# Kernel optimization log

Hardware: AMD Instinct MI355X
Metric: run time of the kernel (lower is better)

The kernel has to match this reference:

```python
import jax, jax.numpy as jnp
import numpy as np

B, T, D, H, L, FF, SPLIT = 2, 4096, 256, 4 * 0 + 8, 4, 1024, 2048
HD = D // H
EPS = 1e-5


def _layernorm(x, s, b):
    mu = jnp.mean(x, axis=-1, keepdims=True)
    var = jnp.mean(jnp.square(x - mu), axis=-1, keepdims=True)
    return (x - mu) * jax.lax.rsqrt(var + EPS) * s + b


def setup_inputs() -> dict:
    key = jax.random.key(0)
    ks = jax.random.split(key, 10)
    sc = 0.02
    inp = {
        "rows": jax.random.normal(ks[0], (B, T, D), jnp.float32),
        "train_target_embeddings": jax.random.normal(ks[1], (B, SPLIT, D), jnp.float32),
        "Wq": sc * jax.random.normal(ks[2], (L, D, D), jnp.float32),
        "bq": jnp.zeros((L, D), jnp.float32),
        "Wk": sc * jax.random.normal(ks[3], (L, D, D), jnp.float32),
        "bk": jnp.zeros((L, D), jnp.float32),
        "Wv": sc * jax.random.normal(ks[4], (L, D, D), jnp.float32),
        "bv": jnp.zeros((L, D), jnp.float32),
        "Wo": sc * jax.random.normal(ks[5], (L, D, D), jnp.float32),
        "bo": jnp.zeros((L, D), jnp.float32),
        "W1": sc * jax.random.normal(ks[6], (L, D, FF), jnp.float32),
        "b1": jnp.zeros((L, FF), jnp.float32),
        "W2": sc * jax.random.normal(ks[7], (L, FF, D), jnp.float32),
        "b2": jnp.zeros((L, D), jnp.float32),
        "ln1_s": jnp.ones((L, D), jnp.float32),
        "ln1_b": jnp.zeros((L, D), jnp.float32),
        "ln2_s": jnp.ones((L, D), jnp.float32),
        "ln2_b": jnp.zeros((L, D), jnp.float32),
        "split": SPLIT,
    }
    return inp


def reference(rows, train_target_embeddings, Wq, bq, Wk, bk, Wv, bv, Wo, bo,
              W1, b1, W2, b2, ln1_s, ln1_b, ln2_s, ln2_b, split):
    # residual add of train target embeddings onto the train rows
    x = rows.at[:, :split, :].add(train_target_embeddings)
    t = x.shape[1]
    # allowed mask: every query can see all train columns; test queries also see themselves
    key_is_train = jnp.arange(t) < split                      # [T]
    allowed = key_is_train[None, :] | jnp.eye(t, dtype=bool)  # [T,T]
    neg = jnp.asarray(-1e9, x.dtype)
    scale = 1.0 / np.sqrt(HD)
    n_layers = Wq.shape[0]
    for l in range(n_layers):
        # multi-head attention with structured mask
        q = (x @ Wq[l] + bq[l]).reshape(x.shape[0], t, H, HD)
        k = (x @ Wk[l] + bk[l]).reshape(x.shape[0], t, H, HD)
        v = (x @ Wv[l] + bv[l]).reshape(x.shape[0], t, H, HD)
        logits = jnp.einsum('bqhd,bkhd->bhqk', q, k) * scale
        logits = jnp.where(allowed[None, None], logits, neg)
        attn = jax.nn.softmax(logits, axis=-1)
        o = jnp.einsum('bhqk,bkhd->bqhd', attn, v).reshape(x.shape[0], t, D)
        x = _layernorm(x + (o @ Wo[l] + bo[l]), ln1_s[l], ln1_b[l])
        # feed-forward
        h = jax.nn.gelu(x @ W1[l] + b1[l])
        x = _layernorm(x + (h @ W2[l] + b2[l]), ln2_s[l], ln2_b[l])
    return x
```

## Files before the change

### kernel.cpp

```cpp
#include <hip/hip_runtime.h>
#include <cstdint>
#include <cstddef>

#define TSEQ 4096
#define BATCH 2
#define DIM 256
#define NHEAD 8
#define HDIM 32
#define NLAYER 4
#define FFDIM 1024
#define SPLITN 2048
#define MROWS (BATCH * TSEQ)

#define QSCALE 0.2550784545f

typedef __attribute__((ext_vector_type(4))) float f32x4;
typedef __attribute__((ext_vector_type(8))) short bf16x8;

__device__ __forceinline__ short f2bf(float f) {
  union { float f; uint32_t u; } v; v.f = f;
  uint32_t r = v.u + 0x7fffu + ((v.u >> 16) & 1u);
  return (short)(r >> 16);
}

__device__ __forceinline__ float fast_exp2(float x) {
#if __has_builtin(__builtin_amdgcn_exp2f)
  return __builtin_amdgcn_exp2f(x);
#else
  float r;
  asm volatile("v_exp_f32 %0, %1\n\ts_nop 1" : "=v"(r) : "v"(x));
  return r;
#endif
}

__device__ __forceinline__ uint32_t pack2bf(float a, float b) {
  union { float f; uint32_t u; } ua, ub; ua.f = a; ub.f = b;
  return ((ua.u + 0x8000u) >> 16) | ((ub.u + 0x8000u) & 0xffff0000u);
}

__device__ __forceinline__ float gelu_f(float x) {
  float u = 0.7978845608f * x * (1.0f + 0.044715f * x * x);
  u = fminf(fmaxf(u, -20.f), 20.f);
  float e = fast_exp2(2.885390082f * u);
  float t = (e - 1.0f) / (e + 1.0f);
  return 0.5f * x * (1.0f + t);
}

#define AS1 __attribute__((address_space(1)))
#define AS3 __attribute__((address_space(3)))
__device__ __forceinline__ void gload16(const void* g, void* l) {
  __builtin_amdgcn_global_load_lds((AS1 void*)g, (AS3 void*)l, 16, 0, 0);
}

__global__ __launch_bounds__(256) void prep_w(
    const float* __restrict__ Wq, const float* __restrict__ Wk,
    const float* __restrict__ Wv, const float* __restrict__ Wo,
    const float* __restrict__ W1, const float* __restrict__ W2,
    short* __restrict__ qkvT, short* __restrict__ woT,
    short* __restrict__ w1T, short* __restrict__ w2T)
{
  const int NQKV = NLAYER * 768 * DIM;
  const int NO   = NLAYER * DIM * DIM;
  const int NF   = NLAYER * FFDIM * DIM;
  const int total = NQKV + NO + 2 * NF;
  for (int idx = blockIdx.x * 256 + threadIdx.x; idx < total; idx += gridDim.x * 256) {
    if (idx < NQKV) {
      const int l = idx / (768 * DIM);
      const int rem = idx - l * 768 * DIM;
      const int n = rem >> 8, k = rem & 255;
      const float* src = (n < 256) ? Wq : ((n < 512) ? Wk : Wv);
      qkvT[idx] = f2bf(src[((size_t)l * DIM + k) * DIM + (n & 255)]);
    } else if (idx < NQKV + NO) {
      const int j = idx - NQKV;
      const int l = j >> 16;
      const int rem = j & 65535;
      const int n = rem >> 8, k = rem & 255;
      woT[j] = f2bf(Wo[((size_t)l * DIM + k) * DIM + n]);
    } else if (idx < NQKV + NO + NF) {
      const int j = idx - NQKV - NO;
      const int l = j >> 18;
      const int rem = j & 262143;
      const int n = rem >> 8, k = rem & 255;
      w1T[j] = f2bf(W1[((size_t)l * DIM + k) * FFDIM + n]);
    } else {
      const int j = idx - NQKV - NO - NF;
      const int l = j >> 18;
      const int rem = j & 262143;
      const int n = rem >> 10, k = rem & 1023;
      w2T[j] = f2bf(W2[((size_t)l * FFDIM + k) * DIM + n]);
    }
  }
}

__global__ __launch_bounds__(256) void prep_x(
    const float* __restrict__ rows, const float* __restrict__ tte,
    float* __restrict__ xf, short* __restrict__ xb)
{
  const size_t idx = (size_t)blockIdx.x * 256 + threadIdx.x;
  float4 v = ((const float4*)rows)[idx];
  const size_t e = idx * 4;
  const int m = (int)(e >> 8);
  const int d = (int)(e & 255);
  const int t = m & (TSEQ - 1);
  const int bb = m >> 12;
  if (t < SPLITN) {
    const float4 a = ((const float4*)tte)[((size_t)bb * SPLITN + t) * (DIM / 4) + (d >> 2)];
    v.x += a.x; v.y += a.y; v.z += a.z; v.w += a.w;
  }
  ((float4*)xf)[idx] = v;
  short4 pk; pk.x = f2bf(v.x); pk.y = f2bf(v.y); pk.z = f2bf(v.z); pk.w = f2bf(v.w);
  ((short4*)xb)[idx] = pk;
}

#define GBM 128
#define GBN 64
#define GBK 64

template<int EPI>
__global__ __launch_bounds__(256, 4) void gemm_bt(
    const short* __restrict__ A, const short* __restrict__ BT,
    const float* __restrict__ bias0, const float* __restrict__ bias1,
    const float* __restrict__ bias2, void* __restrict__ Cout,
    int M, int N, int K)
{
  __shared__ short As[GBM * GBK];
  __shared__ short Bs[GBN * GBK];
  const int tid = threadIdx.x;
  const int lane = tid & 63;
  const int wave = tid >> 6;
  const int wm = wave & 1, wn = wave >> 1;
  const int col = lane & 15, quad = lane >> 4;

  const short* Ab = A + (size_t)blockIdx.x * GBM * K;
  const short* Bb = BT + (size_t)blockIdx.y * GBN * K;

  const f32x4 fz = {0.f, 0.f, 0.f, 0.f};
  f32x4 acc[4][2];
#pragma unroll
  for (int i = 0; i < 4; ++i)
#pragma unroll
    for (int j = 0; j < 2; ++j) acc[i][j] = fz;

  for (int k0 = 0; k0 < K; k0 += GBK) {
#pragma unroll
    for (int p = 0; p < 4; ++p) {
      int i = p * 256 + tid;
      gload16(Ab + (size_t)(i >> 3) * K + k0 + (i & 7) * 8, &As[i * 8]);
    }
#pragma unroll
    for (int p = 0; p < 2; ++p) {
      int i = p * 256 + tid;
      gload16(Bb + (size_t)(i >> 3) * K + k0 + (i & 7) * 8, &Bs[i * 8]);
    }
    __syncthreads();
#pragma unroll
    for (int ks = 0; ks < GBK; ks += 32) {
      bf16x8 af[4], bfr[2];
#pragma unroll
      for (int tm = 0; tm < 4; ++tm)
        af[tm] = *(const bf16x8*)&As[(wm * 64 + tm * 16 + col) * GBK + ks + quad * 8];
#pragma unroll
      for (int tn = 0; tn < 2; ++tn)
        bfr[tn] = *(const bf16x8*)&Bs[(wn * 32 + tn * 16 + col) * GBK + ks + quad * 8];
#pragma unroll
      for (int tm = 0; tm < 4; ++tm)
#pragma unroll
        for (int tn = 0; tn < 2; ++tn)
          acc[tm][tn] = __builtin_amdgcn_mfma_f32_16x16x32_bf16(af[tm], bfr[tn], acc[tm][tn], 0, 0, 0);
    }
    __syncthreads();
  }

#pragma unroll
  for (int tm = 0; tm < 4; ++tm) {
    const int mbase = blockIdx.x * GBM + wm * 64 + tm * 16 + quad * 4;
#pragma unroll
    for (int tn = 0; tn < 2; ++tn) {
      const int n = blockIdx.y * GBN + wn * 32 + tn * 16 + col;
      float bv;
      if (EPI == 1) bv = (n < 256) ? bias0[n] : ((n < 512) ? bias1[n - 256] : bias2[n - 512]);
      else          bv = bias0[n];
#pragma unroll
      for (int r = 0; r < 4; ++r) {
        float v = acc[tm][tn][r] + bv;
        size_t off = (size_t)(mbase + r) * N + n;
        if (EPI == 1) {
          if (n < 256) v *= QSCALE;
          ((short*)Cout)[off] = f2bf(v);
        } else {
          ((short*)Cout)[off] = f2bf(gelu_f(v));
        }
      }
    }
  }
}

__global__ __launch_bounds__(256, 3) void gemm_ln(
    const short* __restrict__ A, const short* __restrict__ BT,
    const float* __restrict__ bias, const float* __restrict__ xres,
    const float* __restrict__ gs, const float* __restrict__ gb,
    float* __restrict__ xoutf, short* __restrict__ xoutb, int K)
{
  __shared__ short As[32 * 64];
  __shared__ short Bs[256 * 64];
  __shared__ float ssum[4][32], ssq[4][32];
  const int tid = threadIdx.x;
  const int lane = tid & 63;
  const int wave = tid >> 6;
  const int col = lane & 15, quad = lane >> 4;
  const int m0 = blockIdx.x * 32;
  const short* Ab = A + (size_t)m0 * K;

  const f32x4 fz = {0.f, 0.f, 0.f, 0.f};
  f32x4 acc[2][4];
#pragma unroll
  for (int i = 0; i < 2; ++i)
#pragma unroll
    for (int j = 0; j < 4; ++j) acc[i][j] = fz;

  for (int k0 = 0; k0 < K; k0 += 64) {
    gload16(Ab + (size_t)(tid >> 3) * K + k0 + (tid & 7) * 8, &As[tid * 8]);
#pragma unroll
    for (int p = 0; p < 8; ++p) {
      int i = p * 256 + tid;
      gload16(BT + (size_t)(i >> 3) * K + k0 + (i & 7) * 8, &Bs[i * 8]);
    }
    __syncthreads();
#pragma unroll
    for (int ks = 0; ks < 64; ks += 32) {
      bf16x8 af[2], bfr[4];
#pragma unroll
      for (int tm = 0; tm < 2; ++tm)
        af[tm] = *(const bf16x8*)&As[(tm * 16 + col) * 64 + ks + quad * 8];
#pragma unroll
      for (int tn = 0; tn < 4; ++tn)
        bfr[tn] = *(const bf16x8*)&Bs[(wave * 64 + tn * 16 + col) * 64 + ks + quad * 8];
#pragma unroll
      for (int tm = 0; tm < 2; ++tm)
#pragma unroll
        for (int tn = 0; tn < 4; ++tn)
          acc[tm][tn] = __builtin_amdgcn_mfma_f32_16x16x32_bf16(af[tm], bfr[tn], acc[tm][tn], 0, 0, 0);
    }
    __syncthreads();
  }

  const float* resb = xres + (size_t)m0 * DIM;
#pragma unroll
  for (int tn = 0; tn < 4; ++tn) {
    const int n = wave * 64 + tn * 16 + col;
    const float bv = bias[n];
#pragma unroll
    for (int tm = 0; tm < 2; ++tm)
#pragma unroll
      for (int r = 0; r < 4; ++r) {
        const int row = tm * 16 + quad * 4 + r;
        acc[tm][tn][r] += bv + resb[(size_t)row * DIM + n];
      }
  }

#pragma unroll
  for (int tm = 0; tm < 2; ++tm)
#pragma unroll
    for (int r = 0; r < 4; ++r) {
      float s = 0.f, q = 0.f;
#pragma unroll
      for (int tn = 0; tn < 4; ++tn) { const float v = acc[tm][tn][r]; s += v; q += v * v; }
      s += __shfl_xor(s, 1); q += __shfl_xor(q, 1);
      s += __shfl_xor(s, 2); q += __shfl_xor(q, 2);
      s += __shfl_xor(s, 4); q += __shfl_xor(q, 4);
      s += __shfl_xor(s, 8); q += __shfl_xor(q, 8);
      if (col == 0) { const int row = tm * 16 + quad * 4 + r; ssum[wave][row] = s; ssq[wave][row] = q; }
    }
  __syncthreads();
  if (tid < 32) {
    const float S = ssum[0][tid] + ssum[1][tid] + ssum[2][tid] + ssum[3][tid];
    const float Q = ssq[0][tid] + ssq[1][tid] + ssq[2][tid] + ssq[3][tid];
    const float mu = S * (1.0f / DIM);
    const float var = Q * (1.0f / DIM) - mu * mu;
    ssum[0][tid] = mu;
    ssq[0][tid] = rsqrtf(var + 1e-5f);
  }
  __syncthreads();

#pragma unroll
  for (int tm = 0; tm < 2; ++tm)
#pragma unroll
    for (int tn = 0; tn < 4; ++tn) {
      const int n = wave * 64 + tn * 16 + col;
      const float g = gs[n], bb = gb[n];
#pragma unroll
      for (int r = 0; r < 4; ++r) {
        const int row = tm * 16 + quad * 4 + r;
        const float out = (acc[tm][tn][r] - ssum[0][row]) * ssq[0][row] * g + bb;
        xoutf[(size_t)(m0 + row) * DIM + n] = out;
        xoutb[(size_t)(m0 + row) * DIM + n] = f2bf(out);
      }
    }
}

__global__ __launch_bounds__(256) void transpose_v(
    const short* __restrict__ qkv, short* __restrict__ vt)
{
  __shared__ short tile[32][33];
  const int t0 = blockIdx.x * 32;
  const int c0 = blockIdx.y * 32;
  const int b = blockIdx.z;
  const int tx = threadIdx.x & 31, ty = threadIdx.x >> 5;
#pragma unroll
  for (int i = 0; i < 4; ++i) {
    const int t = t0 + ty + i * 8;
    tile[ty + i * 8][tx] = qkv[(size_t)(b * TSEQ + t) * 768 + 512 + c0 + tx];
  }
  __syncthreads();
#pragma unroll
  for (int i = 0; i < 4; ++i) {
    const int c = c0 + ty + i * 8;
    vt[(size_t)(b * DIM + c) * TSEQ + t0 + tx] = tile[tx][ty + i * 8];
  }
}

#define AKT 64
#define KSPL 1024

__global__ __launch_bounds__(256, 4) void attn_kernel(
    const short* __restrict__ qkv, const short* __restrict__ vt,
    float* __restrict__ Opart, float* __restrict__ lpart)
{
  __shared__ short Kbuf[2][AKT * HDIM];
  __shared__ short Vbuf[2][HDIM * AKT];
  __shared__ short Pall[4][32][72];

  const int tid = threadIdx.x;
  const int lane = tid & 63;
  const int wave = tid >> 6;
  const int col = lane & 15, quad = lane >> 4;
  const int bh = blockIdx.y;
  const int b = bh >> 3, h = bh & 7;
  const int hz = blockIdx.z;
  const int q0 = blockIdx.x * 128 + wave * 32;

  short (*P)[72] = Pall[wave];

  const short* qbase = qkv + (size_t)b * TSEQ * 768 + h * HDIM;
  const short* kbase = qbase + 256;
  const short* vtb = vt + (size_t)bh * HDIM * TSEQ;

  const short* ksrc = kbase + (size_t)(hz * KSPL + (tid & 63)) * 768 + (tid >> 6) * 8;
  const short* vsrc = vtb + (size_t)(tid >> 3) * TSEQ + hz * KSPL + (((tid & 7) ^ ((tid >> 3) & 7)) * 8);

  const bf16x8 qf0 = *(const bf16x8*)(qbase + (size_t)(q0 + col) * 768 + quad * 8);
  const bf16x8 qf1 = *(const bf16x8*)(qbase + (size_t)(q0 + 16 + col) * 768 + quad * 8);

  bf16x8 ones;
#pragma unroll
  for (int i = 0; i < 8; ++i) ones[i] = (short)0x3F80;

  const f32x4 fz = {0.f, 0.f, 0.f, 0.f};
  f32x4 o[2][2] = {{fz, fz}, {fz, fz}};
  f32x4 lacc0 = fz, lacc1 = fz;

  gload16(ksrc, &Kbuf[0][tid * 8]);
  gload16(vsrc, &Vbuf[0][tid * 8]);

  int cur = 0;
  for (int t = 0; t < KSPL / AKT; ++t) {
    __syncthreads();
    if (t + 1 < KSPL / AKT) {
      const int kn = (t + 1) * AKT;
      gload16(ksrc + (size_t)kn * 768, &Kbuf[1 - cur][tid * 8]);
      gload16(vsrc + kn, &Vbuf[1 - cur][tid * 8]);
    }
    const short* kb = Kbuf[cur];
    const short* vb = Vbuf[cur];

#pragma unroll
    for (int st = 0; st < 4; ++st) {
      const bf16x8 kf = *(const bf16x8*)&kb[(quad * 64 + st * 16 + col) * 8];
      const f32x4 s0 = __builtin_amdgcn_mfma_f32_16x16x32_bf16(kf, qf0, fz, 0, 0, 0);
      const f32x4 s1 = __builtin_amdgcn_mfma_f32_16x16x32_bf16(kf, qf1, fz, 0, 0, 0);
      uint2 w0, w1;
      w0.x = pack2bf(fast_exp2(s0[0]), fast_exp2(s0[1]));
      w0.y = pack2bf(fast_exp2(s0[2]), fast_exp2(s0[3]));
      w1.x = pack2bf(fast_exp2(s1[0]), fast_exp2(s1[1]));
      w1.y = pack2bf(fast_exp2(s1[2]), fast_exp2(s1[3]));
      *(uint2*)&P[col][st * 16 + quad * 4] = w0;
      *(uint2*)&P[16 + col][st * 16 + quad * 4] = w1;
    }
    asm volatile("s_waitcnt lgkmcnt(0)" ::: "memory");

#pragma unroll
    for (int kh = 0; kh < 2; ++kh) {
      const bf16x8 pf0 = *(const bf16x8*)&P[col][kh * 32 + quad * 8];
      const bf16x8 pf1 = *(const bf16x8*)&P[16 + col][kh * 32 + quad * 8];
#pragma unroll
      for (int hh = 0; hh < 2; ++hh) {
        const int hd = hh * 16 + col;
        const bf16x8 vf = *(const bf16x8*)&vb[hd * AKT + (((kh * 4 + quad) ^ (hd & 7)) * 8)];
        o[0][hh] = __builtin_amdgcn_mfma_f32_16x16x32_bf16(pf0, vf, o[0][hh], 0, 0, 0);
        o[1][hh] = __builtin_amdgcn_mfma_f32_16x16x32_bf16(pf1, vf, o[1][hh], 0, 0, 0);
      }
      lacc0 = __builtin_amdgcn_mfma_f32_16x16x32_bf16(pf0, ones, lacc0, 0, 0, 0);
      lacc1 = __builtin_amdgcn_mfma_f32_16x16x32_bf16(pf1, ones, lacc1, 0, 0, 0);
    }
    cur ^= 1;
  }

  if (hz == 1 && blockIdx.x >= SPLITN / 128) {
#pragma unroll
    for (int qsub = 0; qsub < 2; ++qsub) {
      const int qd = q0 + qsub * 16;
      const bf16x8 qf = qsub ? qf1 : qf0;
      const bf16x8 kf = *(const bf16x8*)(kbase + (size_t)(qd + col) * 768 + quad * 8);
      const f32x4 sd = __builtin_amdgcn_mfma_f32_16x16x32_bf16(kf, qf, fz, 0, 0, 0);
      float pd[4];
#pragma unroll
      for (int r = 0; r < 4; ++r)
        pd[r] = (quad * 4 + r) == col ? fast_exp2(sd[r]) : 0.f;
      uint2 w0, wz; wz.x = 0; wz.y = 0;
      w0.x = pack2bf(pd[0], pd[1]); w0.y = pack2bf(pd[2], pd[3]);
      *(uint2*)&P[qsub * 16 + col][quad * 4] = w0;
      *(uint2*)&P[qsub * 16 + col][16 + quad * 4] = wz;
    }
    asm volatile("s_waitcnt lgkmcnt(0)" ::: "memory");
#pragma unroll
    for (int qsub = 0; qsub < 2; ++qsub) {
      const int qd = q0 + qsub * 16;
      const bf16x8 pf = *(const bf16x8*)&P[qsub * 16 + col][quad * 8];
#pragma unroll
      for (int hh = 0; hh < 2; ++hh) {
        const bf16x8 vf = *(const bf16x8*)(vtb + (size_t)(hh * 16 + col) * TSEQ + qd + quad * 8);
        o[qsub][hh] = __builtin_amdgcn_mfma_f32_16x16x32_bf16(pf, vf, o[qsub][hh], 0, 0, 0);
      }
      if (qsub == 0) lacc0 = __builtin_amdgcn_mfma_f32_16x16x32_bf16(pf, ones, lacc0, 0, 0, 0);
      else           lacc1 = __builtin_amdgcn_mfma_f32_16x16x32_bf16(pf, ones, lacc1, 0, 0, 0);
    }
  }

  float* Ob = Opart + (size_t)hz * MROWS * DIM;
  float* lb = lpart + (size_t)hz * 16 * TSEQ + (size_t)bh * TSEQ;
#pragma unroll
  for (int qsub = 0; qsub < 2; ++qsub) {
    const f32x4 la = qsub ? lacc1 : lacc0;
    const int qq = q0 + qsub * 16 + quad * 4;
    const int rowb = b * TSEQ + qq;
#pragma unroll
    for (int r = 0; r < 4; ++r) {
      if (col == 0) lb[qq + r] = la[r];
#pragma unroll
      for (int hh = 0; hh < 2; ++hh)
        Ob[(size_t)(rowb + r) * DIM + h * HDIM + hh * 16 + col] = o[qsub][hh][r];
    }
  }
}

__global__ __launch_bounds__(256) void attn_combine(
    const float* __restrict__ Opart, const float* __restrict__ lpart,
    short* __restrict__ ob)
{
  const int idx4 = blockIdx.x * 256 + threadIdx.x;
  const int row = idx4 >> 6, d4 = idx4 & 63;
  const int h = d4 >> 3, b = row >> 12, t = row & (TSEQ - 1);
  const int bh = b * 8 + h;
  const float l = lpart[bh * TSEQ + t] + lpart[16 * TSEQ + bh * TSEQ + t];
  const float4 o0 = ((const float4*)Opart)[idx4];
  const float4 o1 = ((const float4*)Opart)[(size_t)MROWS * (DIM / 4) + idx4];
  const float linv = 1.0f / l;
  short4 pk;
  pk.x = f2bf((o0.x + o1.x) * linv);
  pk.y = f2bf((o0.y + o1.y) * linv);
  pk.z = f2bf((o0.z + o1.z) * linv);
  pk.w = f2bf((o0.w + o1.w) * linv);
  ((short4*)ob)[idx4] = pk;
}

extern "C" void kernel_launch(void* const* d_in, const int* in_sizes, int n_in,
                              void* d_out, int out_size, void* d_ws, size_t ws_size,
                              hipStream_t stream)
{
  const float* rows = (const float*)d_in[0];
  const float* tte  = (const float*)d_in[1];
  const float* Wq = (const float*)d_in[2];  const float* bq = (const float*)d_in[3];
  const float* Wk = (const float*)d_in[4];  const float* bk = (const float*)d_in[5];
  const float* Wv = (const float*)d_in[6];  const float* bv = (const float*)d_in[7];
  const float* Wo = (const float*)d_in[8];  const float* bo = (const float*)d_in[9];
  const float* W1 = (const float*)d_in[10]; const float* b1 = (const float*)d_in[11];
  const float* W2 = (const float*)d_in[12]; const float* b2 = (const float*)d_in[13];
  const float* ln1s = (const float*)d_in[14]; const float* ln1b = (const float*)d_in[15];
  const float* ln2s = (const float*)d_in[16]; const float* ln2b = (const float*)d_in[17];

  char* p = (char*)d_ws;
  float* xf   = (float*)p;  p += (size_t)MROWS * DIM * 4;
  short* xb   = (short*)p;  p += (size_t)MROWS * DIM * 2;
  short* qkv  = (short*)p;  p += (size_t)MROWS * 768 * 2;
  short* vtb  = (short*)p;  p += (size_t)BATCH * DIM * TSEQ * 2;
  short* ob   = (short*)p;  p += (size_t)MROWS * DIM * 2;
  short* hb   = (short*)p;  p += (size_t)MROWS * FFDIM * 2;
  float* Opart = (float*)p; p += (size_t)2 * MROWS * DIM * 4;
  float* lpart = (float*)p; p += (size_t)2 * 16 * TSEQ * 4;
  short* qkvT = (short*)p;  p += (size_t)NLAYER * 768 * DIM * 2;
  short* woT  = (short*)p;  p += (size_t)NLAYER * DIM * DIM * 2;
  short* w1T  = (short*)p;  p += (size_t)NLAYER * FFDIM * DIM * 2;
  short* w2T  = (short*)p;  p += (size_t)NLAYER * DIM * FFDIM * 2;

  prep_w<<<2048, 256, 0, stream>>>(Wq, Wk, Wv, Wo, W1, W2, qkvT, woT, w1T, w2T);
  prep_x<<<MROWS * DIM / 4 / 256, 256, 0, stream>>>(rows, tte, xf, xb);

  for (int l = 0; l < NLAYER; ++l) {
    gemm_bt<1><<<dim3(MROWS / GBM, 768 / GBN), 256, 0, stream>>>(
        xb, qkvT + (size_t)l * 768 * DIM, bq + l * DIM, bk + l * DIM, bv + l * DIM,
        qkv, MROWS, 768, DIM);
    transpose_v<<<dim3(TSEQ / 32, DIM / 32, BATCH), 256, 0, stream>>>(qkv, vtb);
    attn_kernel<<<dim3(TSEQ / 128, BATCH * NHEAD, 2), 256, 0, stream>>>(qkv, vtb, Opart, lpart);
    attn_combine<<<MROWS * DIM / 4 / 256, 256, 0, stream>>>(Opart, lpart, ob);
    gemm_ln<<<MROWS / 32, 256, 0, stream>>>(
        ob, woT + (size_t)l * DIM * DIM, bo + l * DIM, xf,
        ln1s + l * DIM, ln1b + l * DIM, xf, xb, DIM);
    gemm_bt<3><<<dim3(MROWS / GBM, FFDIM / GBN), 256, 0, stream>>>(
        xb, w1T + (size_t)l * FFDIM * DIM, b1 + l * FFDIM, nullptr, nullptr,
        hb, MROWS, FFDIM, DIM);
    float* xo = (l == NLAYER - 1) ? (float*)d_out : xf;
    gemm_ln<<<MROWS / 32, 256, 0, stream>>>(
        hb, w2T + (size_t)l * DIM * FFDIM, b2 + l * DIM, xf,
        ln2s + l * DIM, ln2b + l * DIM, xo, xb, FFDIM);
  }
}
```

Before: 530.2 us.

## Fuse attention combine into out-proj GEMM and drop V transpose kernel

Removes the transpose_v and attn_combine kernels. The attention kernel now reads V rows directly from qkv and transposes them into swizzled LDS through a register prefetch. The diagonal test-key term is computed with scalar FMAs instead of an MFMA over transposed V. The out-projection GEMM+LN kernel gets a mode that merges the two split-K partials and normalizes them while loading A into XOR-swizzled LDS. This saves two launches and the round trips through vtb/ob, at the cost of scalar LDS scatter stores for V and a heavier fp32 A load in the GEMM.

Result: faster. 512.4 us (-3.3%).

```diff
diff --git a/kernel.cpp b/kernel.cpp
--- a/kernel.cpp
+++ b/kernel.cpp
@@ -21,6 +21,11 @@
   union { float f; uint32_t u; } v; v.f = f;
   uint32_t r = v.u + 0x7fffu + ((v.u >> 16) & 1u);
   return (short)(r >> 16);
+}
+
+__device__ __forceinline__ float bf2f(short s) {
+  union { uint32_t u; float f; } v; v.u = ((uint32_t)(uint16_t)s) << 16;
+  return v.f;
 }
 
 __device__ __forceinline__ float fast_exp2(float x) {
@@ -195,9 +200,12 @@
   }
 }
 
+template<int MODE>
 __global__ __launch_bounds__(256, 3) void gemm_ln(
-    const short* __restrict__ A, const short* __restrict__ BT,
-    const float* __restrict__ bias, const float* __restrict__ xres,
+    const short* __restrict__ A, const float* __restrict__ Opart,
+    const float* __restrict__ lpart,
+    const short* __restrict__ BT, const float* __restrict__ bias,
+    const float* __restrict__ xres,
     const float* __restrict__ gs, const float* __restrict__ gb,
     float* __restrict__ xoutf, short* __restrict__ xoutb, int K)
 {
@@ -209,7 +217,6 @@
   const int wave = tid >> 6;
   const int col = lane & 15, quad = lane >> 4;
   const int m0 = blockIdx.x * 32;
-  const short* Ab = A + (size_t)m0 * K;
 
   const f32x4 fz = {0.f, 0.f, 0.f, 0.f};
   f32x4 acc[2][4];
@@ -218,8 +225,32 @@
 #pragma unroll
     for (int j = 0; j < 4; ++j) acc[i][j] = fz;
 
+  const int arow = tid >> 3;
+  const int agr  = tid & 7;
+  const int grow = m0 + arow;
+
   for (int k0 = 0; k0 < K; k0 += 64) {
-    gload16(Ab + (size_t)(tid >> 3) * K + k0 + (tid & 7) * 8, &As[tid * 8]);
+    if (MODE == 0) {
+      const bf16x8 av = *(const bf16x8*)(A + (size_t)grow * K + k0 + agr * 8);
+      *(bf16x8*)&As[arow * 64 + ((agr ^ (arow & 7)) * 8)] = av;
+    } else {
+      const int tt = grow & (TSEQ - 1), bb = grow >> 12;
+      const int head = (k0 >> 5) + (agr >= 4 ? 1 : 0);
+      const size_t lidx = (size_t)(bb * 8 + head) * TSEQ + tt;
+      const float l = lpart[lidx] + lpart[(size_t)16 * TSEQ + lidx];
+      const float li = 1.0f / l;
+      const size_t obase = (size_t)grow * DIM + k0 + agr * 8;
+      const float4 a0 = *(const float4*)(Opart + obase);
+      const float4 a1 = *(const float4*)(Opart + obase + 4);
+      const float4 c0 = *(const float4*)(Opart + (size_t)MROWS * DIM + obase);
+      const float4 c1 = *(const float4*)(Opart + (size_t)MROWS * DIM + obase + 4);
+      uint4 w;
+      w.x = pack2bf((a0.x + c0.x) * li, (a0.y + c0.y) * li);
+      w.y = pack2bf((a0.z + c0.z) * li, (a0.w + c0.w) * li);
+      w.z = pack2bf((a1.x + c1.x) * li, (a1.y + c1.y) * li);
+      w.w = pack2bf((a1.z + c1.z) * li, (a1.w + c1.w) * li);
+      *(uint4*)&As[arow * 64 + ((agr ^ (arow & 7)) * 8)] = w;
+    }
 #pragma unroll
     for (int p = 0; p < 8; ++p) {
       int i = p * 256 + tid;
@@ -230,8 +261,11 @@
     for (int ks = 0; ks < 64; ks += 32) {
       bf16x8 af[2], bfr[4];
 #pragma unroll
-      for (int tm = 0; tm < 2; ++tm)
-        af[tm] = *(const bf16x8*)&As[(tm * 16 + col) * 64 + ks + quad * 8];
+      for (int tm = 0; tm < 2; ++tm) {
+        const int row = tm * 16 + col;
+        const int g = (ks >> 3) + quad;
+        af[tm] = *(const bf16x8*)&As[row * 64 + ((g ^ (row & 7)) * 8)];
+      }
 #pragma unroll
       for (int tn = 0; tn < 4; ++tn)
         bfr[tn] = *(const bf16x8*)&Bs[(wave * 64 + tn * 16 + col) * 64 + ks + quad * 8];
@@ -298,37 +332,18 @@
     }
 }
 
-__global__ __launch_bounds__(256) void transpose_v(
-    const short* __restrict__ qkv, short* __restrict__ vt)
-{
-  __shared__ short tile[32][33];
-  const int t0 = blockIdx.x * 32;
-  const int c0 = blockIdx.y * 32;
-  const int b = blockIdx.z;
-  const int tx = threadIdx.x & 31, ty = threadIdx.x >> 5;
-#pragma unroll
-  for (int i = 0; i < 4; ++i) {
-    const int t = t0 + ty + i * 8;
-    tile[ty + i * 8][tx] = qkv[(size_t)(b * TSEQ + t) * 768 + 512 + c0 + tx];
-  }
-  __syncthreads();
-#pragma unroll
-  for (int i = 0; i < 4; ++i) {
-    const int c = c0 + ty + i * 8;
-    vt[(size_t)(b * DIM + c) * TSEQ + t0 + tx] = tile[tx][ty + i * 8];
-  }
-}
-
 #define AKT 64
 #define KSPL 1024
+#define NKT (KSPL / AKT)
 
 __global__ __launch_bounds__(256, 4) void attn_kernel(
-    const short* __restrict__ qkv, const short* __restrict__ vt,
+    const short* __restrict__ qkv,
     float* __restrict__ Opart, float* __restrict__ lpart)
 {
   __shared__ short Kbuf[2][AKT * HDIM];
   __shared__ short Vbuf[2][HDIM * AKT];
   __shared__ short Pall[4][32][72];
+  __shared__ float Pdiag[4][16];
 
   const int tid = threadIdx.x;
   const int lane = tid & 63;
@@ -343,10 +358,12 @@
 
   const short* qbase = qkv + (size_t)b * TSEQ * 768 + h * HDIM;
   const short* kbase = qbase + 256;
-  const short* vtb = vt + (size_t)bh * HDIM * TSEQ;
+  const short* vcol  = qbase + 512;
 
   const short* ksrc = kbase + (size_t)(hz * KSPL + (tid & 63)) * 768 + (tid >> 6) * 8;
-  const short* vsrc = vtb + (size_t)(tid >> 3) * TSEQ + hz * KSPL + (((tid & 7) ^ ((tid >> 3) & 7)) * 8);
+  const int vkey = tid & 63, vhg = tid >> 6;
+  const int va = vkey >> 3, vb8 = vkey & 7;
+  const short* vsrc = vcol + (size_t)(hz * KSPL + vkey) * 768 + vhg * 8;
 
   const bf16x8 qf0 = *(const bf16x8*)(qbase + (size_t)(q0 + col) * 768 + quad * 8);
   const bf16x8 qf1 = *(const bf16x8*)(qbase + (size_t)(q0 + 16 + col) * 768 + quad * 8);
@@ -357,18 +374,26 @@
 
   const f32x4 fz = {0.f, 0.f, 0.f, 0.f};
   f32x4 o[2][2] = {{fz, fz}, {fz, fz}};
-  f32x4 lacc0 = fz, lacc1 = fz;
+  f32x4 lacc[2] = {fz, fz};
 
   gload16(ksrc, &Kbuf[0][tid * 8]);
-  gload16(vsrc, &Vbuf[0][tid * 8]);
+  {
+    const bf16x8 v0 = *(const bf16x8*)vsrc;
+#pragma unroll
+    for (int j = 0; j < 8; ++j)
+      Vbuf[0][(vhg * 8 + j) * 64 + ((va ^ j) * 8) + vb8] = v0[j];
+  }
+  bf16x8 vnext = *(const bf16x8*)(vsrc + (size_t)AKT * 768);
 
   int cur = 0;
-  for (int t = 0; t < KSPL / AKT; ++t) {
+  for (int t = 0; t < NKT; ++t) {
     __syncthreads();
-    if (t + 1 < KSPL / AKT) {
-      const int kn = (t + 1) * AKT;
-      gload16(ksrc + (size_t)kn * 768, &Kbuf[1 - cur][tid * 8]);
-      gload16(vsrc + kn, &Vbuf[1 - cur][tid * 8]);
+    if (t + 1 < NKT) {
+      gload16(ksrc + (size_t)(t + 1) * AKT * 768, &Kbuf[1 - cur][tid * 8]);
+#pragma unroll
+      for (int j = 0; j < 8; ++j)
+        Vbuf[1 - cur][(vhg * 8 + j) * 64 + ((va ^ j) * 8) + vb8] = vnext[j];
+      if (t + 2 < NKT) vnext = *(const bf16x8*)(vsrc + (size_t)(t + 2) * AKT * 768);
     }
     const short* kb = Kbuf[cur];
     const short* vb = Vbuf[cur];
@@ -399,8 +424,8 @@
         o[0][hh] = __builtin_amdgcn_mfma_f32_16x16x32_bf16(pf0, vf, o[0][hh], 0, 0, 0);
         o[1][hh] = __builtin_amdgcn_mfma_f32_16x16x32_bf16(pf1, vf, o[1][hh], 0, 0, 0);
       }
-      lacc0 = __builtin_amdgcn_mfma_f32_16x16x32_bf16(pf0, ones, lacc0, 0, 0, 0);
-      lacc1 = __builtin_amdgcn_mfma_f32_16x16x32_bf16(pf1, ones, lacc1, 0, 0, 0);
+      lacc[0] = __builtin_amdgcn_mfma_f32_16x16x32_bf16(pf0, ones, lacc[0], 0, 0, 0);
+      lacc[1] = __builtin_amdgcn_mfma_f32_16x16x32_bf16(pf1, ones, lacc[1], 0, 0, 0);
     }
     cur ^= 1;
   }
@@ -412,27 +437,22 @@
       const bf16x8 qf = qsub ? qf1 : qf0;
       const bf16x8 kf = *(const bf16x8*)(kbase + (size_t)(qd + col) * 768 + quad * 8);
       const f32x4 sd = __builtin_amdgcn_mfma_f32_16x16x32_bf16(kf, qf, fz, 0, 0, 0);
-      float pd[4];
+      float ps = 0.f;
 #pragma unroll
       for (int r = 0; r < 4; ++r)
-        pd[r] = (quad * 4 + r) == col ? fast_exp2(sd[r]) : 0.f;
-      uint2 w0, wz; wz.x = 0; wz.y = 0;
-      w0.x = pack2bf(pd[0], pd[1]); w0.y = pack2bf(pd[2], pd[3]);
-      *(uint2*)&P[qsub * 16 + col][quad * 4] = w0;
-      *(uint2*)&P[qsub * 16 + col][16 + quad * 4] = wz;
-    }
-    asm volatile("s_waitcnt lgkmcnt(0)" ::: "memory");
-#pragma unroll
-    for (int qsub = 0; qsub < 2; ++qsub) {
-      const int qd = q0 + qsub * 16;
-      const bf16x8 pf = *(const bf16x8*)&P[qsub * 16 + col][quad * 8];
-#pragma unroll
-      for (int hh = 0; hh < 2; ++hh) {
-        const bf16x8 vf = *(const bf16x8*)(vtb + (size_t)(hh * 16 + col) * TSEQ + qd + quad * 8);
-        o[qsub][hh] = __builtin_amdgcn_mfma_f32_16x16x32_bf16(pf, vf, o[qsub][hh], 0, 0, 0);
+        if (quad * 4 + r == col) ps = fast_exp2(sd[r]);
+      if (quad == (col >> 2)) Pdiag[wave][col] = ps;
+      asm volatile("s_waitcnt lgkmcnt(0)" ::: "memory");
+      const f32x4 pv = *(const f32x4*)&Pdiag[wave][quad * 4];
+#pragma unroll
+      for (int r = 0; r < 4; ++r) {
+        lacc[qsub][r] += pv[r];
+        const size_t vrow = (size_t)(qd + quad * 4 + r) * 768;
+#pragma unroll
+        for (int hh = 0; hh < 2; ++hh)
+          o[qsub][hh][r] += pv[r] * bf2f(vcol[vrow + hh * 16 + col]);
       }
-      if (qsub == 0) lacc0 = __builtin_amdgcn_mfma_f32_16x16x32_bf16(pf, ones, lacc0, 0, 0, 0);
-      else           lacc1 = __builtin_amdgcn_mfma_f32_16x16x32_bf16(pf, ones, lacc1, 0, 0, 0);
+      asm volatile("s_waitcnt lgkmcnt(0)" ::: "memory");
     }
   }
 
@@ -440,7 +460,7 @@
   float* lb = lpart + (size_t)hz * 16 * TSEQ + (size_t)bh * TSEQ;
 #pragma unroll
   for (int qsub = 0; qsub < 2; ++qsub) {
-    const f32x4 la = qsub ? lacc1 : lacc0;
+    const f32x4 la = lacc[qsub];
     const int qq = q0 + qsub * 16 + quad * 4;
     const int rowb = b * TSEQ + qq;
 #pragma unroll
@@ -451,26 +471,6 @@
         Ob[(size_t)(rowb + r) * DIM + h * HDIM + hh * 16 + col] = o[qsub][hh][r];
     }
   }
-}
-
-__global__ __launch_bounds__(256) void attn_combine(
-    const float* __restrict__ Opart, const float* __restrict__ lpart,
-    short* __restrict__ ob)
-{
-  const int idx4 = blockIdx.x * 256 + threadIdx.x;
-  const int row = idx4 >> 6, d4 = idx4 & 63;
-  const int h = d4 >> 3, b = row >> 12, t = row & (TSEQ - 1);
-  const int bh = b * 8 + h;
-  const float l = lpart[bh * TSEQ + t] + lpart[16 * TSEQ + bh * TSEQ + t];
-  const float4 o0 = ((const float4*)Opart)[idx4];
-  const float4 o1 = ((const float4*)Opart)[(size_t)MROWS * (DIM / 4) + idx4];
-  const float linv = 1.0f / l;
-  short4 pk;
-  pk.x = f2bf((o0.x + o1.x) * linv);
-  pk.y = f2bf((o0.y + o1.y) * linv);
-  pk.z = f2bf((o0.z + o1.z) * linv);
-  pk.w = f2bf((o0.w + o1.w) * linv);
-  ((short4*)ob)[idx4] = pk;
 }
 
 extern "C" void kernel_launch(void* const* d_in, const int* in_sizes, int n_in,
@@ -492,8 +492,6 @@
   float* xf   = (float*)p;  p += (size_t)MROWS * DIM * 4;
   short* xb   = (short*)p;  p += (size_t)MROWS * DIM * 2;
   short* qkv  = (short*)p;  p += (size_t)MROWS * 768 * 2;
-  short* vtb  = (short*)p;  p += (size_t)BATCH * DIM * TSEQ * 2;
-  short* ob   = (short*)p;  p += (size_t)MROWS * DIM * 2;
   short* hb   = (short*)p;  p += (size_t)MROWS * FFDIM * 2;
   float* Opart = (float*)p; p += (size_t)2 * MROWS * DIM * 4;
   float* lpart = (float*)p; p += (size_t)2 * 16 * TSEQ * 4;
@@ -509,18 +507,16 @@
     gemm_bt<1><<<dim3(MROWS / GBM, 768 / GBN), 256, 0, stream>>>(
         xb, qkvT + (size_t)l * 768 * DIM, bq + l * DIM, bk + l * DIM, bv + l * DIM,
         qkv, MROWS, 768, DIM);
-    transpose_v<<<dim3(TSEQ / 32, DIM / 32, BATCH), 256, 0, stream>>>(qkv, vtb);
-    attn_kernel<<<dim3(TSEQ / 128, BATCH * NHEAD, 2), 256, 0, stream>>>(qkv, vtb, Opart, lpart);
-    attn_combine<<<MROWS * DIM / 4 / 256, 256, 0, stream>>>(Opart, lpart, ob);
-    gemm_ln<<<MROWS / 32, 256, 0, stream>>>(
-        ob, woT + (size_t)l * DIM * DIM, bo + l * DIM, xf,
+    attn_kernel<<<dim3(TSEQ / 128, BATCH * NHEAD, 2), 256, 0, stream>>>(qkv, Opart, lpart);
+    gemm_ln<1><<<MROWS / 32, 256, 0, stream>>>(
+        nullptr, Opart, lpart, woT + (size_t)l * DIM * DIM, bo + l * DIM, xf,
         ln1s + l * DIM, ln1b + l * DIM, xf, xb, DIM);
     gemm_bt<3><<<dim3(MROWS / GBM, FFDIM / GBN), 256, 0, stream>>>(
         xb, w1T + (size_t)l * FFDIM * DIM, b1 + l * FFDIM, nullptr, nullptr,
         hb, MROWS, FFDIM, DIM);
     float* xo = (l == NLAYER - 1) ? (float*)d_out : xf;
-    gemm_ln<<<MROWS / 32, 256, 0, stream>>>(
-        hb, w2T + (size_t)l * DIM * FFDIM, b2 + l * DIM, xf,
-        ln2s + l * DIM, ln2b + l * DIM, xo, xb, FFDIM);
-  }
-}
+    gemm_ln<0><<<MROWS / 32, 256, 0, stream>>>(
+        hb, nullptr, nullptr, w2T + (size_t)l * DIM * FFDIM,
+        b2 + l * DIM, xf, ln2s + l * DIM, ln2b + l * DIM, xo, xb, FFDIM);
+  }
+}
```
